# Optimization experiments

Hardware: AMD Instinct MI355X
Metric: run time of the kernel (lower is better)

Reference implementation:

```python
import jax, jax.numpy as jnp
import numpy as np

N_NODES = 100000
N_EDGES = 1600000
DIM = 64

def setup_inputs() -> dict:
    key = jax.random.key(0)
    k1, k2, k3 = jax.random.split(key, 3)
    x = jax.random.normal(k1, (N_NODES, DIM), dtype=jnp.float32)
    edge_index = jax.random.randint(k2, (2, N_EDGES), 0, N_NODES, dtype=jnp.int64)
    edge_weight = jax.random.uniform(k3, (N_EDGES,), dtype=jnp.float32)
    return {"x": x, "edge_index": edge_index, "edge_weight": edge_weight}

def reference(x, edge_index, edge_weight):
    # out[row] += x[col] * edge_weight  (edge-weighted gather + scatter-add)
    row, col = edge_index[0], edge_index[1]
    messages = x[col] * edge_weight[:, None]            # [E, dim]
    out = jax.ops.segment_sum(messages, row, num_segments=x.shape[0])  # [N, dim]
    return out
```

## Files before the change

### kernel.cpp

```cpp
#include <hip/hip_runtime.h>
#include <hip/hip_fp16.h>
#include <stdint.h>


typedef unsigned long long ull;
typedef int   v4i __attribute__((ext_vector_type(4)));
typedef float v4f __attribute__((ext_vector_type(4)));
typedef unsigned char  uchar;

#define RB      64
#define CAP     1280
#define CHUNK   4096
#define EPT     8
#define SLOTS   48
#define BPAD    16
#define OVF_CAP 65536
#define NSBP    32
#define SBROWS  4096

__device__ __forceinline__ unsigned short f2bf(float f) {
    union { float f; unsigned int u; } c;
    c.f = f;
    unsigned int lsb = (c.u >> 16) & 1u;
    c.u += 0x7fffu + lsb;
    return (unsigned short)(c.u >> 16);
}
__device__ __forceinline__ float bf2f(unsigned short u) {
    union { unsigned int u; float f; } c;
    c.u = ((unsigned int)u) << 16;
    return c.f;
}
__device__ __forceinline__ float unpack_w(unsigned v) {
    return __half2float(__ushort_as_half((unsigned short)((v & 0x7fffu) << 1)));
}

__global__ __launch_bounds__(512) void prep(
    const int* __restrict__ ei, const float* __restrict__ ew,
    int* __restrict__ bcnt1, ull* __restrict__ seg1, int cap1,
    int* __restrict__ ovf_cnt, int3* __restrict__ ovf, int E, int nbin,
    const float* __restrict__ x, unsigned short* __restrict__ xb, int n4)
{
    __shared__ int hist[NSBP];
    __shared__ int lstart[NSBP];
    __shared__ int gbase[NSBP];
    __shared__ ull sorted[CHUNK];
    int t = threadIdx.x;

    if ((int)blockIdx.x >= nbin) {
        int i0 = ((int)blockIdx.x - nbin) * 4096 + t;
#pragma unroll
        for (int k = 0; k < 8; ++k) {
            int i = i0 + k * 512;
            if (i < n4) {
                v4f v = ((const v4f*)x)[i];
                ushort4 o;
                o.x = f2bf(v.x); o.y = f2bf(v.y);
                o.z = f2bf(v.z); o.w = f2bf(v.w);
                ((ushort4*)xb)[i] = o;
            }
        }
        return;
    }

    if (t < NSBP) hist[t] = 0;
    __syncthreads();

    int e0   = blockIdx.x * CHUNK;
    int nval = E - e0; if (nval > CHUNK) nval = CHUNK;
    bool al4 = ((E & 3) == 0);

    int   rk[EPT];
    uchar sb[EPT];
    ull   cw[EPT];
    bool  vd[EPT];
#pragma unroll
    for (int j = 0; j < EPT / 4; ++j) {
        int eb = e0 + (j * 512 + t) * 4;
        v4i r4, c4; v4f w4;
        if (al4 && eb + 3 < E) {
            r4 = *(const v4i*)(ei + eb);
            c4 = *(const v4i*)(ei + E + eb);
            w4 = *(const v4f*)(ew + eb);
        } else {
#pragma unroll
            for (int u = 0; u < 4; ++u) {
                int e = eb + u;
                r4[u] = e < E ? ei[e] : 0;
                c4[u] = e < E ? ei[E + e] : 0;
                w4[u] = e < E ? ew[e] : 0.f;
            }
        }
#pragma unroll
        for (int u = 0; u < 4; ++u) {
            int idx = j * 4 + u;
            int e = eb + u;
            vd[idx] = e < E;
            int b = r4[u] >> 12;
            rk[idx] = vd[idx] ? atomicAdd(&hist[b], 1) : 0;
            sb[idx] = (uchar)b;
            unsigned hw = __half_as_ushort(__float2half(w4[u]));
            cw[idx] = ((ull)hw << 48) | ((ull)(unsigned)r4[u] << 24) |
                      (ull)(unsigned)c4[u];
        }
    }
    __syncthreads();

    if (t < 32) {
        int h = hist[t];
        gbase[t] = h ? atomicAdd(&bcnt1[t * BPAD], h) : 0;
        int s = h;
#pragma unroll
        for (int off = 1; off < 32; off <<= 1) {
            int o = __shfl_up(s, off);
            if (t >= off) s += o;
        }
        lstart[t] = s - h;
    }
    __syncthreads();

#pragma unroll
    for (int j = 0; j < EPT; ++j) {
        if (!vd[j]) continue;
        sorted[lstart[sb[j]] + rk[j]] = cw[j];
    }
    __syncthreads();

    for (int i = t; i < nval; i += 512) {
        ull e = sorted[i];
        int b = (int)((e >> 24) & 0x1FFFF) >> 12;
        int loc = gbase[b] + (i - lstart[b]);
        if (loc < cap1) {
            seg1[(size_t)b * cap1 + loc] = e;
        } else {
            int o = atomicAdd(ovf_cnt, 1);
            if (o < OVF_CAP)
                ovf[o] = make_int3((int)((e >> 24) & 0x1FFFF),
                                   (int)(e & 0x1FFFF),
                                   __float_as_int(__half2float(
                                       __ushort_as_half((unsigned short)(e >> 48)))));
        }
    }
}

__global__ __launch_bounds__(512) void bin2(
    const ull* __restrict__ seg1, int cap1, const int* __restrict__ bcnt1,
    int* __restrict__ bcnt, ull* __restrict__ seg2,
    int* __restrict__ ovf_cnt, int3* __restrict__ ovf, int chpersb)
{
    __shared__ int hist[64];
    __shared__ int lstart[64];
    __shared__ int gbase[64];
    __shared__ ull sorted[CHUNK];
    int t  = threadIdx.x;
    int sb = blockIdx.x / chpersb;
    int ch = blockIdx.x % chpersb;

    int cnt1 = bcnt1[sb * BPAD];
    if (cnt1 > cap1) cnt1 = cap1;
    int s0 = ch * CHUNK;
    int nval = cnt1 - s0;
    if (nval <= 0) return;
    if (nval > CHUNK) nval = CHUNK;

    if (t < 64) hist[t] = 0;
    __syncthreads();

    const ull* base = seg1 + (size_t)sb * cap1 + s0;

    int   rk[EPT];
    uchar fb[EPT];
    ull   cw[EPT];
    bool  vd[EPT];
#pragma unroll
    for (int j = 0; j < EPT; ++j) {
        int i = t + j * 512;
        vd[j] = i < nval;
        ull e = vd[j] ? base[i] : 0;
        int row = (int)((e >> 24) & 0x1FFFF);
        int f = (row >> 6) & 63;
        rk[j] = vd[j] ? atomicAdd(&hist[f], 1) : 0;
        fb[j] = (uchar)f;
        cw[j] = e;
    }
    __syncthreads();

    if (t < 64) {
        int h = hist[t];
        int fbg = sb * 64 + t;
        gbase[t] = h ? atomicAdd(&bcnt[fbg * BPAD], h) : 0;
        int s = h;
#pragma unroll
        for (int off = 1; off < 64; off <<= 1) {
            int o = __shfl_up(s, off);
            if (t >= off) s += o;
        }
        lstart[t] = s - h;
    }
    __syncthreads();

#pragma unroll
    for (int j = 0; j < EPT; ++j) {
        if (!vd[j]) continue;
        sorted[lstart[fb[j]] + rk[j]] = cw[j];
    }
    __syncthreads();

    for (int i = t; i < nval; i += 512) {
        ull e = sorted[i];
        int row = (int)((e >> 24) & 0x1FFFF);
        int f = (row >> 6) & 63;
        int loc = gbase[f] + (i - lstart[f]);
        int fbg = sb * 64 + f;
        if (loc < CAP) {
            ull hw = (e >> 48) & 0xFFFF;
            seg2[(size_t)fbg * CAP + loc] =
                (hw << 32) | ((ull)(unsigned)(row & 63) << 17) |
                (e & 0x1FFFF);
        } else {
            int o = atomicAdd(ovf_cnt, 1);
            if (o < OVF_CAP)
                ovf[o] = make_int3(row, (int)(e & 0x1FFFF),
                                   __float_as_int(__half2float(
                                       __ushort_as_half((unsigned short)(e >> 48)))));
        }
    }
}

template <bool BF>
__global__ __launch_bounds__(256, 8) void bucket_acc(
    const void* __restrict__ xv, const ull* __restrict__ seg2,
    const int* __restrict__ bcnt, float* __restrict__ out,
    int* __restrict__ ovf_cnt, int3* __restrict__ ovf, int N)
{
    __shared__ int      cur[RB];
    __shared__ unsigned tile[RB * SLOTS];
    int t = threadIdx.x;
    int g = blockIdx.x;
    if (t < RB) cur[t] = 0;
    __syncthreads();

    int c = bcnt[g * BPAD];
    if (c > CAP) c = CAP;
    const ull* b8 = seg2 + (size_t)g * CAP;

    for (int i = t; i < c; i += 256) {
        ull e = b8[i];
        int rl = (int)((e >> 17) & 63);
        unsigned p4 = ((unsigned)(e & 0x1FFFF) << 15) |
                      ((unsigned)(e >> 33) & 0x7FFF);
        int pos = atomicAdd(&cur[rl], 1);
        if (pos < SLOTS) {
            tile[rl * SLOTS + pos] = p4;
        } else {
            int o = atomicAdd(ovf_cnt, 1);
            if (o < OVF_CAP)
                ovf[o] = make_int3(g * RB + rl, (int)(p4 >> 15),
                                   __float_as_int(unpack_w(p4)));
        }
    }
    __syncthreads();

    int wid  = t >> 6;
    int lane = t & 63;
    const unsigned short* xh = (const unsigned short*)xv;
    const float*          xf = (const float*)xv;

    for (int k = 0; k < 16; ++k) {
        int r   = wid * 16 + k;
        int row = g * RB + r;
        if (row >= N) break;
        int cc = cur[r];
        if (cc > SLOTS) cc = SLOTS;
        const unsigned* tb = &tile[r * SLOTS];

        float acc = 0.0f;
        int p = 0;
        for (; p + 8 <= cc; p += 8) {
            unsigned a[8]; float xr[8];
#pragma unroll
            for (int i = 0; i < 8; ++i) a[i] = tb[p + i];
#pragma unroll
            for (int i = 0; i < 8; ++i) {
                size_t off = (((size_t)(a[i] >> 15)) << 6) + lane;
                xr[i] = BF ? bf2f(xh[off]) : xf[off];
            }
#pragma unroll
            for (int i = 0; i < 8; ++i)
                acc = fmaf(xr[i], unpack_w(a[i]), acc);
        }
        if (p < cc) {
            unsigned a[8]; float xr[8], w[8];
#pragma unroll
            for (int i = 0; i < 8; ++i) {
                int q = p + i;
                bool valid = q < cc;
                if (!valid) q = cc - 1;
                a[i] = tb[q];
                w[i] = valid ? unpack_w(a[i]) : 0.0f;
            }
#pragma unroll
            for (int i = 0; i < 8; ++i) {
                size_t off = (((size_t)(a[i] >> 15)) << 6) + lane;
                xr[i] = BF ? bf2f(xh[off]) : xf[off];
            }
#pragma unroll
            for (int i = 0; i < 8; ++i) acc = fmaf(xr[i], w[i], acc);
        }
        __builtin_nontemporal_store(acc, out + (((size_t)row) << 6) + lane);
    }
}

template <bool BF>
__global__ __launch_bounds__(256) void ovf_apply(
    const void* __restrict__ xv, const int* __restrict__ ovf_cnt,
    const int3* __restrict__ ovf, float* __restrict__ out)
{
    int n = *ovf_cnt;
    if (n > OVF_CAP) n = OVF_CAP;
    int wid  = (blockIdx.x * 256 + threadIdx.x) >> 6;
    int lane = threadIdx.x & 63;
    int nw   = gridDim.x * 4;
    for (int o = wid; o < n; o += nw) {
        int3 tt = ovf[o];
        float w = __int_as_float(tt.z);
        size_t off = (((size_t)tt.y) << 6) + lane;
        float x = BF ? bf2f(((const unsigned short*)xv)[off])
                     : ((const float*)xv)[off];
        atomicAdd(&out[(((size_t)tt.x) << 6) + lane], x * w);
    }
}

__global__ __launch_bounds__(256) void scatter_edges(
    const float* __restrict__ x, const int* __restrict__ ei,
    const float* __restrict__ ew, float* __restrict__ out, int E)
{
    long long idx = (long long)blockIdx.x * 256 + threadIdx.x;
    int e = (int)(idx >> 4);
    if (e >= E) return;
    int j = (int)(idx & 15);
    int row = ei[e];
    int col = ei[E + e];
    float w = ew[e];
    v4f v = *(const v4f*)(x + (((size_t)col) << 6) + (j << 2));
    float* op = out + (((size_t)row) << 6) + (j << 2);
    atomicAdd(op + 0, v.x * w);
    atomicAdd(op + 1, v.y * w);
    atomicAdd(op + 2, v.z * w);
    atomicAdd(op + 3, v.w * w);
}

extern "C" void kernel_launch(void* const* d_in, const int* in_sizes, int n_in,
                              void* d_out, int out_size, void* d_ws, size_t ws_size,
                              hipStream_t stream) {
    const float* x  = (const float*)d_in[0];
    const int*   ei = (const int*)d_in[1];
    const float* ew = (const float*)d_in[2];
    float*       out = (float*)d_out;

    int E = in_sizes[2];
    int N = out_size / 64;
    int NB  = (N + RB - 1) / RB;
    int NSB = (N + SBROWS - 1) / SBROWS;

    long long mean1 = (long long)E * SBROWS / (N > 0 ? N : 1);
    int cap1 = (int)(mean1 + mean1 / 20 + CHUNK);
    cap1 = (cap1 + 1023) & ~1023;
    int chpersb = (cap1 + CHUNK - 1) / CHUNK;

    size_t bcnt_base = (size_t)NSBP * BPAD;
    size_t ovfc_base = bcnt_base + (size_t)NB * BPAD;
    size_t ovf_base  = (ovfc_base + 1 + 3) & ~(size_t)3;
    size_t xb_base   = (ovf_base + 3 * (size_t)OVF_CAP + 3) & ~(size_t)3;
    size_t seg1_base = (xb_base + (size_t)N * 32 + 1) & ~(size_t)1;
    size_t seg2_base = seg1_base + (size_t)NSB * cap1 * 2;
    size_t need      = (seg2_base + (size_t)NB * CAP * 2) * 4;

    int nbin  = (E + CHUNK - 1) / CHUNK;
    int n4    = (N * 64) / 4;
    int nconv = (n4 + CHUNK - 1) / CHUNK;

    if (ws_size >= need && N <= (1 << 17)) {
        int* w32 = (int*)d_ws;
        int* bcnt1   = w32;
        int* bcnt    = w32 + bcnt_base;
        int* ovf_cnt = w32 + ovfc_base;
        int3* ovf    = (int3*)(w32 + ovf_base);
        unsigned short* xb = (unsigned short*)(w32 + xb_base);
        ull* seg1 = (ull*)(w32 + seg1_base);
        ull* seg2 = (ull*)(w32 + seg2_base);

        (void)hipMemsetAsync(w32, 0,
            (bcnt_base + (size_t)NB * BPAD + 2) * sizeof(int), stream);

        prep<<<nbin + nconv, 512, 0, stream>>>(
            ei, ew, bcnt1, seg1, cap1, ovf_cnt, ovf, E, nbin, x, xb, n4);
        bin2<<<NSB * chpersb, 512, 0, stream>>>(
            seg1, cap1, bcnt1, bcnt, seg2, ovf_cnt, ovf, chpersb);
        bucket_acc<true><<<NB, 256, 0, stream>>>(
            xb, seg2, bcnt, out, ovf_cnt, ovf, N);
        ovf_apply<true><<<64, 256, 0, stream>>>(xb, ovf_cnt, ovf, out);
    } else {
        (void)hipMemsetAsync(out, 0, (size_t)out_size * sizeof(float), stream);
        long long threads = (long long)E * 16;
        scatter_edges<<<(int)((threads + 255) / 256), 256, 0, stream>>>(
            x, ei, ew, out, E);
    }
}
```

Baseline: 163.6 us.

## Split per-row gather into two column-half phases for cache locality

Each row's edge slots are partitioned by whether the source column lies in the lower or upper half of the node range. Each wave then processes all 16 of its rows for the lower half before moving to the upper half, keeping 16 accumulators in registers. The aim is to shrink the working set of x touched at any moment across the GPU so gathers hit L2/MALL more often. The cost is that per-half capacity is 24 slots, so rows with a skewed column split overflow to the global overflow path sooner, and register pressure rises.

```diff
diff --git a/kernel.cpp b/kernel.cpp
--- a/kernel.cpp
+++ b/kernel.cpp
@@ -13,6 +13,7 @@
 #define CHUNK   4096
 #define EPT     8
 #define SLOTS   48
+#define HSLOT   24
 #define BPAD    16
 #define OVF_CAP 65536
 #define NSBP    32
@@ -232,13 +233,14 @@
     const int* __restrict__ bcnt, float* __restrict__ out,
     int* __restrict__ ovf_cnt, int3* __restrict__ ovf, int N)
 {
-    __shared__ int      cur[RB];
+    __shared__ int      cur2[RB * 2];
     __shared__ unsigned tile[RB * SLOTS];
     int t = threadIdx.x;
     int g = blockIdx.x;
-    if (t < RB) cur[t] = 0;
-    __syncthreads();
-
+    if (t < RB * 2) cur2[t] = 0;
+    __syncthreads();
+
+    int nhalf = N >> 1;
     int c = bcnt[g * BPAD];
     if (c > CAP) c = CAP;
     const ull* b8 = seg2 + (size_t)g * CAP;
@@ -248,13 +250,15 @@
         int rl = (int)((e >> 17) & 63);
         unsigned p4 = ((unsigned)(e & 0x1FFFF) << 15) |
                       ((unsigned)(e >> 33) & 0x7FFF);
-        int pos = atomicAdd(&cur[rl], 1);
-        if (pos < SLOTS) {
-            tile[rl * SLOTS + pos] = p4;
+        int col = (int)(e & 0x1FFFF);
+        int ph  = col >= nhalf ? 1 : 0;
+        int pos = atomicAdd(&cur2[rl * 2 + ph], 1);
+        if (pos < HSLOT) {
+            tile[rl * SLOTS + ph * HSLOT + pos] = p4;
         } else {
             int o = atomicAdd(ovf_cnt, 1);
             if (o < OVF_CAP)
-                ovf[o] = make_int3(g * RB + rl, (int)(p4 >> 15),
+                ovf[o] = make_int3(g * RB + rl, col,
                                    __float_as_int(unpack_w(p4)));
         }
     }
@@ -265,48 +269,63 @@
     const unsigned short* xh = (const unsigned short*)xv;
     const float*          xf = (const float*)xv;
 
+    float acc[16];
+#pragma unroll
+    for (int k = 0; k < 16; ++k) acc[k] = 0.0f;
+
+#pragma unroll
+    for (int ph = 0; ph < 2; ++ph) {
+#pragma unroll
+        for (int k = 0; k < 16; ++k) {
+            int r   = wid * 16 + k;
+            int row = g * RB + r;
+            if (row >= N) continue;
+            int cc = cur2[r * 2 + ph];
+            if (cc > HSLOT) cc = HSLOT;
+            const unsigned* tb = &tile[r * SLOTS + ph * HSLOT];
+
+            int p = 0;
+            for (; p + 8 <= cc; p += 8) {
+                unsigned a[8]; float xr[8];
+#pragma unroll
+                for (int i = 0; i < 8; ++i) a[i] = tb[p + i];
+#pragma unroll
+                for (int i = 0; i < 8; ++i) {
+                    size_t off = (((size_t)(a[i] >> 15)) << 6) + lane;
+                    xr[i] = BF ? bf2f(xh[off]) : xf[off];
+                }
+#pragma unroll
+                for (int i = 0; i < 8; ++i)
+                    acc[k] = fmaf(xr[i], unpack_w(a[i]), acc[k]);
+            }
+            if (p < cc) {
+                unsigned a[8]; float xr[8], w[8];
+#pragma unroll
+                for (int i = 0; i < 8; ++i) {
+                    int q = p + i;
+                    bool valid = q < cc;
+                    if (!valid) q = cc - 1;
+                    a[i] = tb[q];
+                    w[i] = valid ? unpack_w(a[i]) : 0.0f;
+                }
+#pragma unroll
+                for (int i = 0; i < 8; ++i) {
+                    size_t off = (((size_t)(a[i] >> 15)) << 6) + lane;
+                    xr[i] = BF ? bf2f(xh[off]) : xf[off];
+                }
+#pragma unroll
+                for (int i = 0; i < 8; ++i)
+                    acc[k] = fmaf(xr[i], w[i], acc[k]);
+            }
+        }
+    }
+
+#pragma unroll
     for (int k = 0; k < 16; ++k) {
-        int r   = wid * 16 + k;
-        int row = g * RB + r;
-        if (row >= N) break;
-        int cc = cur[r];
-        if (cc > SLOTS) cc = SLOTS;
-        const unsigned* tb = &tile[r * SLOTS];
-
-        float acc = 0.0f;
-        int p = 0;
-        for (; p + 8 <= cc; p += 8) {
-            unsigned a[8]; float xr[8];
-#pragma unroll
-            for (int i = 0; i < 8; ++i) a[i] = tb[p + i];
-#pragma unroll
-            for (int i = 0; i < 8; ++i) {
-                size_t off = (((size_t)(a[i] >> 15)) << 6) + lane;
-                xr[i] = BF ? bf2f(xh[off]) : xf[off];
-            }
-#pragma unroll
-            for (int i = 0; i < 8; ++i)
-                acc = fmaf(xr[i], unpack_w(a[i]), acc);
-        }
-        if (p < cc) {
-            unsigned a[8]; float xr[8], w[8];
-#pragma unroll
-            for (int i = 0; i < 8; ++i) {
-                int q = p + i;
-                bool valid = q < cc;
-                if (!valid) q = cc - 1;
-                a[i] = tb[q];
-                w[i] = valid ? unpack_w(a[i]) : 0.0f;
-            }
-#pragma unroll
-            for (int i = 0; i < 8; ++i) {
-                size_t off = (((size_t)(a[i] >> 15)) << 6) + lane;
-                xr[i] = BF ? bf2f(xh[off]) : xf[off];
-            }
-#pragma unroll
-            for (int i = 0; i < 8; ++i) acc = fmaf(xr[i], w[i], acc);
-        }
-        __builtin_nontemporal_store(acc, out + (((size_t)row) << 6) + lane);
+        int row = g * RB + wid * 16 + k;
+        if (row < N)
+            __builtin_nontemporal_store(acc[k],
+                out + (((size_t)row) << 6) + lane);
     }
 }
 
```

Measured after the change: 172.4 us. 1.05x slower.
